# Optimization experiments

Hardware: AMD Instinct MI355X
Metric: run time of the kernel (lower is better)

Reference implementation:

```python
import jax, jax.numpy as jnp
import numpy as np

BATCH, DIM, REPS = 4096, 2048, 8


def setup_inputs() -> dict:
    key = jax.random.key(0)
    ks = jax.random.split(key, 6)
    x = jax.random.normal(ks[0], (BATCH, DIM), jnp.float32)
    theta = 0.5 * jax.random.normal(ks[1], (DIM, REPS + 1, 2), jnp.float32)
    preacts_weight = 1.0 + 0.1 * jax.random.normal(ks[2], (DIM, REPS), jnp.float32)
    preacts_bias = 0.1 * jax.random.normal(ks[3], (DIM, REPS), jnp.float32)
    postact_weights = 1.0 + 0.1 * jax.random.normal(ks[4], (DIM,), jnp.float32)
    postact_bias = 0.1 * jax.random.normal(ks[5], (DIM,), jnp.float32)
    return dict(x=x, theta=theta, preacts_weight=preacts_weight,
                preacts_bias=preacts_bias, postact_weights=postact_weights,
                postact_bias=postact_bias)


def _rz(psi, ang):
    # RZ = diag(exp(-i*ang/2), exp(+i*ang/2)); ang broadcasts over (b, dim)
    ph = jnp.exp(ang * (-0.5j))  # complex64
    return jnp.stack([psi[..., 0] * ph, psi[..., 1] * jnp.conj(ph)], axis=-1)


def _ry(psi, ang):
    # RY = [[cos, -sin], [sin, cos]] with half-angle
    c = jnp.cos(0.5 * ang)
    s = jnp.sin(0.5 * ang)
    a, b = psi[..., 0], psi[..., 1]
    return jnp.stack([c * a - s * b, s * a + c * b], axis=-1)


def reference(x, theta, preacts_weight, preacts_bias, postact_weights, postact_bias):
    reps = theta.shape[1] - 1
    batch, dim = x.shape
    # encoded angles per rep: (reps, b, dim)
    enc = preacts_weight.T[:, None, :] * x[None] + preacts_bias.T[:, None, :]
    # |0> then Hadamard -> (1/sqrt2)(|0> + |1>) per (batch, dim) qubit
    inv_sqrt2 = jnp.asarray(1.0 / np.sqrt(2.0), jnp.complex64)
    psi0 = jnp.full((batch, dim, 2), inv_sqrt2, jnp.complex64)
    th0 = theta[:, :reps, 0].T  # (reps, dim)
    th1 = theta[:, :reps, 1].T  # (reps, dim)

    def step(psi, xs):
        t0, t1, e = xs
        psi = _rz(psi, t0)   # trainable RZ, (dim,) broadcast over batch
        psi = _ry(psi, t1)   # trainable RY
        psi = _rz(psi, e)    # data re-uploading RZ, (b, dim)
        return psi, None

    psi, _ = jax.lax.scan(step, psi0, (th0, th1, enc))
    psi = _rz(psi, theta[:, reps, 0])
    psi = _ry(psi, theta[:, reps, 1])
    # <Z> = |psi_0|^2 - |psi_1|^2, real float32
    z = (psi[..., 0].real ** 2 + psi[..., 0].imag ** 2) - \
        (psi[..., 1].real ** 2 + psi[..., 1].imag ** 2)
    return z * postact_weights + postact_bias
```

## Files before the change

kernel.cpp:

```cpp
#include <hip/hip_runtime.h>

constexpr int BATCH = 4096;
constexpr int DIM   = 2048;
constexpr int REPS  = 8;
constexpr float INV2PI = 0.15915494309189535f;

constexpr int TPB   = 256;
constexpr int GRIDX = DIM / TPB;
constexpr int GRIDY = 256;
constexpr int BPB   = BATCH / GRIDY;
constexpr int ILP   = 4;

constexpr int K_XI = 0, K_YI = 1, K_ZI = 2, K_CY = 3, K_SY = 11,
              K_WR = 19, K_BR = 27, K_PW = 35, K_PB = 36, K_N = 37;

__global__ void daruan_setup(const float* __restrict__ theta,
                             const float* __restrict__ paw,
                             const float* __restrict__ pab,
                             const float* __restrict__ postw,
                             const float* __restrict__ postb,
                             float* __restrict__ tab)
{
    const int d = blockIdx.x * blockDim.x + threadIdx.x;
    if (d >= DIM) return;
    const float* th = theta + (size_t)d * (REPS + 1) * 2;

    const float t00 = th[0] * INV2PI;
    const float X0  = __builtin_amdgcn_cosf(t00);
    const float Y0  = __builtin_amdgcn_sinf(t00);
    const float t10 = th[1] * INV2PI;
    const float cy0 = __builtin_amdgcn_cosf(t10);
    const float sy0 = __builtin_amdgcn_sinf(t10);
    tab[K_XI * DIM + d] = X0 * cy0;
    tab[K_YI * DIM + d] = Y0;
    tab[K_ZI * DIM + d] = -X0 * sy0;

#pragma unroll
    for (int r = 1; r <= REPS; ++r) {
        const float t1 = th[2 * r + 1] * INV2PI;
        tab[(K_CY + r - 1) * DIM + d] = __builtin_amdgcn_cosf(t1);
        tab[(K_SY + r - 1) * DIM + d] = __builtin_amdgcn_sinf(t1);
    }
#pragma unroll
    for (int j = 0; j < REPS; ++j) {
        tab[(K_WR + j) * DIM + d] = paw[(size_t)d * REPS + j] * INV2PI;
        tab[(K_BR + j) * DIM + d] = (pab[(size_t)d * REPS + j] + th[2 * (j + 1)]) * INV2PI;
    }
    tab[K_PW * DIM + d] = postw[d];
    tab[K_PB * DIM + d] = postb[d];
}

__global__ __launch_bounds__(TPB, 8)
void daruan_main(const float* __restrict__ x,
                 const float* __restrict__ tab,
                 float* __restrict__ out)
{
    const int d = blockIdx.x * TPB + threadIdx.x;

    const float Xi = tab[K_XI * DIM + d];
    const float Yi = tab[K_YI * DIM + d];
    const float Zi = tab[K_ZI * DIM + d];
    float cy[REPS], sy[REPS], wr[REPS], br[REPS];
#pragma unroll
    for (int k = 0; k < REPS; ++k) {
        cy[k] = tab[(K_CY + k) * DIM + d];
        sy[k] = tab[(K_SY + k) * DIM + d];
        wr[k] = tab[(K_WR + k) * DIM + d];
        br[k] = tab[(K_BR + k) * DIM + d];
    }
    const float pw = tab[K_PW * DIM + d];
    const float pb = tab[K_PB * DIM + d];

    const int bbase = blockIdx.y * BPB;

#pragma unroll 1
    for (int bb = 0; bb < BPB; bb += ILP) {
        float xv[ILP];
#pragma unroll
        for (int i = 0; i < ILP; ++i)
            xv[i] = x[(size_t)(bbase + bb + i) * DIM + d];

        float X[ILP], Y[ILP], Z[ILP];

#pragma unroll
        for (int i = 0; i < ILP; ++i) {
            const float e  = wr[0] * xv[i] + br[0];
            const float ce = __builtin_amdgcn_cosf(e);
            const float se = __builtin_amdgcn_sinf(e);
            X[i] = Xi * ce - Yi * se;
            Y[i] = Xi * se + Yi * ce;
            Z[i] = Zi;
        }

#pragma unroll
        for (int r = 1; r < REPS; ++r) {
#pragma unroll
            for (int i = 0; i < ILP; ++i) {
                const float Xb = X[i] * cy[r - 1] + Z[i] * sy[r - 1];
                const float Zb = Z[i] * cy[r - 1] - X[i] * sy[r - 1];
                const float e  = wr[r] * xv[i] + br[r];
                const float ce = __builtin_amdgcn_cosf(e);
                const float se = __builtin_amdgcn_sinf(e);
                X[i] = Xb * ce - Y[i] * se;
                if (r < REPS - 1)
                    Y[i] = Xb * se + Y[i] * ce;
                Z[i] = Zb;
            }
        }

#pragma unroll
        for (int i = 0; i < ILP; ++i) {
            const float Zf = Z[i] * cy[REPS - 1] - X[i] * sy[REPS - 1];
            out[(size_t)(bbase + bb + i) * DIM + d] = Zf * pw + pb;
        }
    }
}

extern "C" void kernel_launch(void* const* d_in, const int* in_sizes, int n_in,
                              void* d_out, int out_size, void* d_ws, size_t ws_size,
                              hipStream_t stream) {
    const float* x     = (const float*)d_in[0];
    const float* theta = (const float*)d_in[1];
    const float* paw   = (const float*)d_in[2];
    const float* pab   = (const float*)d_in[3];
    const float* postw = (const float*)d_in[4];
    const float* postb = (const float*)d_in[5];
    float* out = (float*)d_out;
    float* tab = (float*)d_ws;

    daruan_setup<<<dim3(DIM / 64), dim3(64), 0, stream>>>(theta, paw, pab, postw, postb, tab);
    daruan_main<<<dim3(GRIDX, GRIDY), dim3(TPB), 0, stream>>>(x, tab, out);
}
```

Before: 36.25 us.

## Fuse parameter setup into main kernel with LDS staging and prefetched x loads

Drops the separate setup kernel and its workspace table. Each block now stages theta, pre-activation weights and biases through shared memory with padded pitches so the global reads coalesce, then computes the per-dimension constants itself. The main loop moves to ILP 8 with half as many y-blocks and software-prefetches the next chunk of x while the current one is computed. This saves a kernel launch and the table round-trip, but every block repeats the setup trig work and register pressure rises, with launch bounds lowered to 4.

```diff
diff --git a/kernel.cpp b/kernel.cpp
--- a/kernel.cpp
+++ b/kernel.cpp
@@ -5,100 +5,105 @@
 constexpr int REPS  = 8;
 constexpr float INV2PI = 0.15915494309189535f;
 
-constexpr int TPB   = 256;
-constexpr int GRIDX = DIM / TPB;
-constexpr int GRIDY = 256;
-constexpr int BPB   = BATCH / GRIDY;
-constexpr int ILP   = 4;
+constexpr int TPB    = 256;
+constexpr int GRIDX  = DIM / TPB;
+constexpr int GRIDY  = 128;
+constexpr int BPB    = BATCH / GRIDY;
+constexpr int ILP    = 8;
+constexpr int NCHUNK = BPB / ILP;
 
-constexpr int K_XI = 0, K_YI = 1, K_ZI = 2, K_CY = 3, K_SY = 11,
-              K_WR = 19, K_BR = 27, K_PW = 35, K_PB = 36, K_N = 37;
+constexpr int TH_PITCH  = 19;
+constexpr int PW_PITCH  = 9;
+constexpr int LDS_FLOATS = TPB * TH_PITCH;
 
-__global__ void daruan_setup(const float* __restrict__ theta,
-                             const float* __restrict__ paw,
-                             const float* __restrict__ pab,
-                             const float* __restrict__ postw,
-                             const float* __restrict__ postb,
-                             float* __restrict__ tab)
+__global__ __launch_bounds__(TPB, 4)
+void daruan_kernel(const float* __restrict__ x,
+                   const float* __restrict__ theta,
+                   const float* __restrict__ paw,
+                   const float* __restrict__ pab,
+                   const float* __restrict__ postw,
+                   const float* __restrict__ postb,
+                   float* __restrict__ out)
 {
-    const int d = blockIdx.x * blockDim.x + threadIdx.x;
-    if (d >= DIM) return;
-    const float* th = theta + (size_t)d * (REPS + 1) * 2;
+    __shared__ float lds[LDS_FLOATS];
+    const int t = threadIdx.x;
+    const int d = blockIdx.x * TPB + t;
 
-    const float t00 = th[0] * INV2PI;
-    const float X0  = __builtin_amdgcn_cosf(t00);
-    const float Y0  = __builtin_amdgcn_sinf(t00);
-    const float t10 = th[1] * INV2PI;
-    const float cy0 = __builtin_amdgcn_cosf(t10);
-    const float sy0 = __builtin_amdgcn_sinf(t10);
-    tab[K_XI * DIM + d] = X0 * cy0;
-    tab[K_YI * DIM + d] = Y0;
-    tab[K_ZI * DIM + d] = -X0 * sy0;
+    {
+        const float* gth = theta + (size_t)blockIdx.x * TPB * 18;
+#pragma unroll
+        for (int p = 0; p < 18; ++p) {
+            const int idx = p * TPB + t;
+            lds[(idx / 18) * TH_PITCH + (idx % 18)] = gth[idx];
+        }
+    }
+    __syncthreads();
 
+    float cy[REPS], sy[REPS], th0n[REPS];
+    float Xi, Yi, Zi;
+    {
+        const float* th_l = lds + t * TH_PITCH;
+        const float t00 = th_l[0] * INV2PI;
+        const float X0  = __builtin_amdgcn_cosf(t00);
+        const float Y0  = __builtin_amdgcn_sinf(t00);
+        const float t10 = th_l[1] * INV2PI;
+        const float c10 = __builtin_amdgcn_cosf(t10);
+        const float s10 = __builtin_amdgcn_sinf(t10);
+        Xi = X0 * c10; Yi = Y0; Zi = -X0 * s10;
 #pragma unroll
-    for (int r = 1; r <= REPS; ++r) {
-        const float t1 = th[2 * r + 1] * INV2PI;
-        tab[(K_CY + r - 1) * DIM + d] = __builtin_amdgcn_cosf(t1);
-        tab[(K_SY + r - 1) * DIM + d] = __builtin_amdgcn_sinf(t1);
+        for (int k = 0; k < REPS; ++k) {
+            const float t1 = th_l[2 * k + 3] * INV2PI;
+            cy[k] = __builtin_amdgcn_cosf(t1);
+            sy[k] = __builtin_amdgcn_sinf(t1);
+            th0n[k] = th_l[2 * k + 2];
+        }
     }
+    __syncthreads();
+
+    {
+        const float* gpw = paw + (size_t)blockIdx.x * TPB * REPS;
+        const float* gpb = pab + (size_t)blockIdx.x * TPB * REPS;
 #pragma unroll
-    for (int j = 0; j < REPS; ++j) {
-        tab[(K_WR + j) * DIM + d] = paw[(size_t)d * REPS + j] * INV2PI;
-        tab[(K_BR + j) * DIM + d] = (pab[(size_t)d * REPS + j] + th[2 * (j + 1)]) * INV2PI;
+        for (int p = 0; p < 8; ++p) {
+            const int idx = p * TPB + t;
+            const int row = idx / 8, col = idx % 8;
+            lds[row * PW_PITCH + col] = gpw[idx];
+            lds[TPB * PW_PITCH + row * PW_PITCH + col] = gpb[idx];
+        }
     }
-    tab[K_PW * DIM + d] = postw[d];
-    tab[K_PB * DIM + d] = postb[d];
-}
+    __syncthreads();
 
-__global__ __launch_bounds__(TPB, 8)
-void daruan_main(const float* __restrict__ x,
-                 const float* __restrict__ tab,
-                 float* __restrict__ out)
-{
-    const int d = blockIdx.x * TPB + threadIdx.x;
-
-    const float Xi = tab[K_XI * DIM + d];
-    const float Yi = tab[K_YI * DIM + d];
-    const float Zi = tab[K_ZI * DIM + d];
-    float cy[REPS], sy[REPS], wr[REPS], br[REPS];
+    float wr[REPS], br[REPS];
 #pragma unroll
     for (int k = 0; k < REPS; ++k) {
-        cy[k] = tab[(K_CY + k) * DIM + d];
-        sy[k] = tab[(K_SY + k) * DIM + d];
-        wr[k] = tab[(K_WR + k) * DIM + d];
-        br[k] = tab[(K_BR + k) * DIM + d];
+        wr[k] = lds[t * PW_PITCH + k] * INV2PI;
+        br[k] = (lds[TPB * PW_PITCH + t * PW_PITCH + k] + th0n[k]) * INV2PI;
     }
-    const float pw = tab[K_PW * DIM + d];
-    const float pb = tab[K_PB * DIM + d];
+    const float pw = postw[d];
+    const float pb = postb[d];
 
     const int bbase = blockIdx.y * BPB;
+    const float* xp = x + (size_t)bbase * DIM + d;
+    float* op = out + (size_t)bbase * DIM + d;
 
-#pragma unroll 1
-    for (int bb = 0; bb < BPB; bb += ILP) {
-        float xv[ILP];
-#pragma unroll
-        for (int i = 0; i < ILP; ++i)
-            xv[i] = x[(size_t)(bbase + bb + i) * DIM + d];
-
+    auto compute_store = [&](const float (&xvv)[ILP], int cc) {
         float X[ILP], Y[ILP], Z[ILP];
-
 #pragma unroll
         for (int i = 0; i < ILP; ++i) {
-            const float e  = wr[0] * xv[i] + br[0];
+            const float e  = wr[0] * xvv[i] + br[0];
             const float ce = __builtin_amdgcn_cosf(e);
             const float se = __builtin_amdgcn_sinf(e);
             X[i] = Xi * ce - Yi * se;
             Y[i] = Xi * se + Yi * ce;
             Z[i] = Zi;
         }
-
 #pragma unroll
         for (int r = 1; r < REPS; ++r) {
 #pragma unroll
             for (int i = 0; i < ILP; ++i) {
                 const float Xb = X[i] * cy[r - 1] + Z[i] * sy[r - 1];
                 const float Zb = Z[i] * cy[r - 1] - X[i] * sy[r - 1];
-                const float e  = wr[r] * xv[i] + br[r];
+                const float e  = wr[r] * xvv[i] + br[r];
                 const float ce = __builtin_amdgcn_cosf(e);
                 const float se = __builtin_amdgcn_sinf(e);
                 X[i] = Xb * ce - Y[i] * se;
@@ -107,13 +112,28 @@
                 Z[i] = Zb;
             }
         }
-
 #pragma unroll
         for (int i = 0; i < ILP; ++i) {
             const float Zf = Z[i] * cy[REPS - 1] - X[i] * sy[REPS - 1];
-            out[(size_t)(bbase + bb + i) * DIM + d] = Zf * pw + pb;
+            op[(size_t)(cc * ILP + i) * DIM] = Zf * pw + pb;
         }
+    };
+
+    float xv[ILP];
+#pragma unroll
+    for (int i = 0; i < ILP; ++i) xv[i] = xp[(size_t)i * DIM];
+
+#pragma unroll 1
+    for (int cc = 0; cc < NCHUNK - 1; ++cc) {
+        float xn[ILP];
+#pragma unroll
+        for (int i = 0; i < ILP; ++i)
+            xn[i] = xp[(size_t)((cc + 1) * ILP + i) * DIM];
+        compute_store(xv, cc);
+#pragma unroll
+        for (int i = 0; i < ILP; ++i) xv[i] = xn[i];
     }
+    compute_store(xv, NCHUNK - 1);
 }
 
 extern "C" void kernel_launch(void* const* d_in, const int* in_sizes, int n_in,
@@ -126,8 +146,7 @@
     const float* postw = (const float*)d_in[4];
     const float* postb = (const float*)d_in[5];
     float* out = (float*)d_out;
-    float* tab = (float*)d_ws;
 
-    daruan_setup<<<dim3(DIM / 64), dim3(64), 0, stream>>>(theta, paw, pab, postw, postb, tab);
-    daruan_main<<<dim3(GRIDX, GRIDY), dim3(TPB), 0, stream>>>(x, tab, out);
+    daruan_kernel<<<dim3(GRIDX, GRIDY), dim3(TPB), 0, stream>>>(
+        x, theta, paw, pab, postw, postb, out);
 }
```

Result: faster. 33.03 us (-8.9%).
